# Performance work log

Measured on AMD Instinct MI355X. Metric: run time of the kernel, lower is better.

## Reference

```python
import jax, jax.numpy as jnp
import numpy as np

HUGE = 1e9  # stand-in for ops.HUGE_INT


def setup_inputs() -> dict:
    key = jax.random.key(0)
    ks = jax.random.split(key, 8)
    B, Q, K = 8, 128, 256
    Dq = Dk = Dv = H = 512
    query = jax.random.normal(ks[0], (B, Q, Dq), dtype=jnp.float32)
    k_ = jax.random.normal(ks[1], (B, K, Dk), dtype=jnp.float32)
    value = jax.random.normal(ks[2], (B, K, Dv), dtype=jnp.float32)
    mask = jax.random.randint(ks[3], (B, K), 0, 2, dtype=jnp.int32)
    # FFN params: linear1 (Dq+Dk -> H, bias), linear2 (H -> 1, no bias)
    W1 = jax.random.normal(ks[4], (Dq + Dk, H), dtype=jnp.float32) * 0.05
    b1 = jax.random.normal(ks[5], (H,), dtype=jnp.float32) * 0.05
    w2 = jax.random.normal(ks[6], (H, 1), dtype=jnp.float32) * 0.05
    return {"query": query, "key": k_, "value": value, "mask": mask,
            "W1": W1, "b1": b1, "w2": w2}


def reference(query, key, value, mask, W1, b1, w2):
    # Additive (FFN) attention. Original tiles query/key into [B, Q*K, Dq+Dk]
    # and applies linear1; concat@W1 is separable, so we project q and k
    # separately and broadcast-add (same math, no tiled concat tensor).
    Dq = query.shape[-1]
    Wq, Wk = W1[:Dq], W1[Dq:]
    q_proj = jnp.einsum('bqd,dh->bqh', query, Wq)   # [B,Q,H]
    k_proj = jnp.einsum('bkd,dh->bkh', key, Wk)     # [B,K,H]
    hidden = jnp.tanh(q_proj[:, :, None, :] + k_proj[:, None, :, :] + b1)  # [B,Q,K,H]
    scores = jnp.einsum('bqkh,h->bqk', hidden, w2[:, 0])  # [B,Q,K]
    # padding mask fill BEFORE scaling, matching the original op order
    scores = jnp.where(mask[:, None, :] != 0, -HUGE, scores)
    scores = scores / jnp.sqrt(jnp.float32(key.shape[-1]))
    attn_weights = jax.nn.softmax(scores, axis=-1)
    attn_vec = jnp.einsum('bqk,bkv->bqv', attn_weights, value)  # dropout=0 at eval
    return attn_vec, attn_weights
```

## Files before the change

### kernel.cpp

```cpp
#include <hip/hip_runtime.h>
#include <hip/hip_bf16.h>

#define B_ 8
#define Q_ 128
#define K_ 256
#define D_ 512
#define TWOLOG2E 2.8853900817779268f
#define SCALE 0.044194173824159216f
#define L2E 1.4426950408889634f
#define MASKVAL (-44194173.824159216f)

typedef __attribute__((ext_vector_type(8))) short frag8;
typedef __attribute__((ext_vector_type(4))) float f32x4;

__device__ __forceinline__ float fexp2(float x) {
  float r;
  asm("v_exp_f32 %0, %1" : "=v"(r) : "v"(x));
  return r;
}
__device__ __forceinline__ float frcp(float x) {
  float r;
  asm("v_rcp_f32 %0, %1" : "=v"(r) : "v"(x));
  return r;
}
__device__ __forceinline__ unsigned f2bf_u(float x) {
  unsigned u = __float_as_uint(x);
  return (u + 0x7FFFu + ((u >> 16) & 1u)) >> 16;
}
__device__ __forceinline__ unsigned short f2bf(float x) {
  return (unsigned short)f2bf_u(x);
}
__device__ __forceinline__ unsigned packbf(float lo, float hi) {
  return f2bf_u(lo) | (f2bf_u(hi) << 16);
}

__global__ __launch_bounds__(256) void gemm_kernel(
    const float* __restrict__ query, const float* __restrict__ key,
    const float* __restrict__ W1, const float* __restrict__ b1,
    float* __restrict__ qp, float* __restrict__ kpbT) {
  __shared__ short As[32 * 64];
  __shared__ short Bs[64 * 72];
  const int t = threadIdx.x;
  const int m0 = blockIdx.y * 32;
  const int n0 = blockIdx.x * 64;
  const bool is_k = (m0 >= B_ * Q_);
  const float* X = is_k ? key : query;
  const int xrow0 = is_k ? (m0 - B_ * Q_) : m0;
  const float* Wb = W1 + (is_k ? (size_t)D_ * D_ : 0);

  const int am = t >> 3;
  const int ac = t & 7;
  const float* gA = X + (size_t)(xrow0 + am) * D_ + ac * 8;
  short* aw = As + am * 64 + ((ac ^ (am & 7)) * 8);

  const int prow = t >> 4;
  const int n4 = (t & 15) * 4;
  const float* gB = Wb + n0 + n4;

  const int l = t & 63;
  const int w = t >> 6;
  const int lr = l & 15;
  const int kg = l >> 4;
  const int key8 = lr & 7;
  int aoff[2][2], boff[2];
#pragma unroll
  for (int kk = 0; kk < 2; ++kk) {
    const int cposA = ((kg + kk * 4) ^ key8) * 8;
#pragma unroll
    for (int mt = 0; mt < 2; ++mt) aoff[mt][kk] = (mt * 16 + lr) * 64 + cposA;
    boff[kk] = (w * 16 + lr) * 72 + (kg + kk * 4) * 8;
  }

  f32x4 acc[2];
  acc[0] = (f32x4){0.f, 0.f, 0.f, 0.f};
  acc[1] = (f32x4){0.f, 0.f, 0.f, 0.f};

  for (int k0 = 0; k0 < D_; k0 += 64) {
    float4 a0 = *(const float4*)(gA + k0);
    float4 a1 = *(const float4*)(gA + k0 + 4);
    float4 w00 = *(const float4*)(gB + (size_t)(k0 + 2 * prow) * D_);
    float4 w01 = *(const float4*)(gB + (size_t)(k0 + 2 * prow + 1) * D_);
    float4 w10 = *(const float4*)(gB + (size_t)(k0 + 2 * prow + 32) * D_);
    float4 w11 = *(const float4*)(gB + (size_t)(k0 + 2 * prow + 33) * D_);
    __syncthreads();
    {
      union { frag8 f; unsigned short u[8]; } av;
      av.u[0] = f2bf(a0.x); av.u[1] = f2bf(a0.y); av.u[2] = f2bf(a0.z); av.u[3] = f2bf(a0.w);
      av.u[4] = f2bf(a1.x); av.u[5] = f2bf(a1.y); av.u[6] = f2bf(a1.z); av.u[7] = f2bf(a1.w);
      *(frag8*)aw = av.f;
    }
    {
      float lo0[4] = {w00.x, w00.y, w00.z, w00.w};
      float hi0[4] = {w01.x, w01.y, w01.z, w01.w};
      float lo1[4] = {w10.x, w10.y, w10.z, w10.w};
      float hi1[4] = {w11.x, w11.y, w11.z, w11.w};
#pragma unroll
      for (int j = 0; j < 4; ++j) {
        *(unsigned*)(Bs + (n4 + j) * 72 + 2 * prow) = packbf(lo0[j], hi0[j]);
        *(unsigned*)(Bs + (n4 + j) * 72 + 2 * (prow + 16)) = packbf(lo1[j], hi1[j]);
      }
    }
    __syncthreads();
#pragma unroll
    for (int kk = 0; kk < 2; ++kk) {
      frag8 bf = *(const frag8*)(Bs + boff[kk]);
#pragma unroll
      for (int mt = 0; mt < 2; ++mt) {
        frag8 af = *(const frag8*)(As + aoff[mt][kk]);
        acc[mt] = __builtin_amdgcn_mfma_f32_16x16x32_bf16(af, bf, acc[mt], 0, 0, 0);
      }
    }
  }

  const int col = n0 + w * 16 + lr;
  if (is_k) {
    const float bc = b1[col];
#pragma unroll
    for (int mt = 0; mt < 2; ++mt) {
      const int krow = m0 - B_ * Q_ + mt * 16 + kg * 4;
      const int bb = krow >> 8;
      const int kk0 = krow & 255;
      float4 v;
      v.x = fexp2((acc[mt][0] + bc) * TWOLOG2E);
      v.y = fexp2((acc[mt][1] + bc) * TWOLOG2E);
      v.z = fexp2((acc[mt][2] + bc) * TWOLOG2E);
      v.w = fexp2((acc[mt][3] + bc) * TWOLOG2E);
      *(float4*)&kpbT[((size_t)bb * D_ + col) * K_ + kk0] = v;
    }
  } else {
#pragma unroll
    for (int mt = 0; mt < 2; ++mt) {
#pragma unroll
      for (int i = 0; i < 4; ++i) {
        const int row = m0 + mt * 16 + kg * 4 + i;
        qp[(size_t)row * D_ + col] = fexp2(acc[mt][i] * TWOLOG2E);
      }
    }
  }
}

__global__ __launch_bounds__(1024) void attn_kernel(
    const float* __restrict__ qp, const float* __restrict__ kpbT,
    const float* __restrict__ value, const int* __restrict__ mask,
    const float* __restrict__ w2,
    float* __restrict__ out_vec, float* __restrict__ out_w) {
  __shared__ float smem_p[16 * 512];
  __shared__ float pw[4 * 256];
  const int bid = blockIdx.x;
  const int b = bid & 7;
  const int q0 = (bid >> 3) * 4;
  const int t = threadIdx.x;
  const int lane = t & 63;
  const int w = __builtin_amdgcn_readfirstlane(t >> 6);
  const int kc = w & 1;
  const int hq = w >> 1;
  const int h0 = hq * 64;

  {
    const float* pk = kpbT + ((size_t)b * D_ + h0) * K_ + kc * 128 + 2 * lane;
    const float* q_0 = qp + (size_t)(b * Q_ + q0 + 0) * D_ + h0;
    const float* q_1 = qp + (size_t)(b * Q_ + q0 + 1) * D_ + h0;
    const float* q_2 = qp + (size_t)(b * Q_ + q0 + 2) * D_ + h0;
    const float* q_3 = qp + (size_t)(b * Q_ + q0 + 3) * D_ + h0;
    const float* w2h = w2 + h0;

    float2 a0 = {0.f, 0.f}, a1 = {0.f, 0.f}, a2 = {0.f, 0.f}, a3 = {0.f, 0.f};
    for (int h = 0; h < 64; h += 8) {
      float2 kv[8];
#pragma unroll
      for (int j = 0; j < 8; ++j) kv[j] = *(const float2*)&pk[(size_t)(h + j) * K_];
      float4 e0a = *(const float4*)(q_0 + h), e0b = *(const float4*)(q_0 + h + 4);
      float4 e1a = *(const float4*)(q_1 + h), e1b = *(const float4*)(q_1 + h + 4);
      float4 e2a = *(const float4*)(q_2 + h), e2b = *(const float4*)(q_2 + h + 4);
      float4 e3a = *(const float4*)(q_3 + h), e3b = *(const float4*)(q_3 + h + 4);
      float4 wa = *(const float4*)(w2h + h), wb = *(const float4*)(w2h + h + 4);
      float E0[8] = {e0a.x, e0a.y, e0a.z, e0a.w, e0b.x, e0b.y, e0b.z, e0b.w};
      float E1[8] = {e1a.x, e1a.y, e1a.z, e1a.w, e1b.x, e1b.y, e1b.z, e1b.w};
      float E2[8] = {e2a.x, e2a.y, e2a.z, e2a.w, e2b.x, e2b.y, e2b.z, e2b.w};
      float E3[8] = {e3a.x, e3a.y, e3a.z, e3a.w, e3b.x, e3b.y, e3b.z, e3b.w};
      float WV[8] = {wa.x, wa.y, wa.z, wa.w, wb.x, wb.y, wb.z, wb.w};
#pragma unroll
      for (int j = 0; j < 8; ++j) {
        a0.x = fmaf(WV[j], frcp(fmaf(E0[j], kv[j].x, 1.f)), a0.x);
        a0.y = fmaf(WV[j], frcp(fmaf(E0[j], kv[j].y, 1.f)), a0.y);
        a1.x = fmaf(WV[j], frcp(fmaf(E1[j], kv[j].x, 1.f)), a1.x);
        a1.y = fmaf(WV[j], frcp(fmaf(E1[j], kv[j].y, 1.f)), a1.y);
        a2.x = fmaf(WV[j], frcp(fmaf(E2[j], kv[j].x, 1.f)), a2.x);
        a2.y = fmaf(WV[j], frcp(fmaf(E2[j], kv[j].y, 1.f)), a2.y);
        a3.x = fmaf(WV[j], frcp(fmaf(E3[j], kv[j].x, 1.f)), a3.x);
        a3.y = fmaf(WV[j], frcp(fmaf(E3[j], kv[j].y, 1.f)), a3.y);
      }
    }
    *(float2*)&smem_p[w * 512 + 0 * 128 + 2 * lane] = a0;
    *(float2*)&smem_p[w * 512 + 1 * 128 + 2 * lane] = a1;
    *(float2*)&smem_p[w * 512 + 2 * 128 + 2 * lane] = a2;
    *(float2*)&smem_p[w * 512 + 3 * 128 + 2 * lane] = a3;
  }
  __syncthreads();

  if (w < 4) {
    const int q = w;
    float sw = 0.f;
#pragma unroll
    for (int m = 0; m < 8; ++m) sw += w2[lane + 64 * m];
#pragma unroll
    for (int off = 32; off; off >>= 1) sw += __shfl_xor(sw, off);

    float s[4];
#pragma unroll
    for (int r = 0; r < 4; ++r) {
      const int kcc = r >> 1;
      const int off = (r & 1) * 64 + lane;
      float p = 0.f;
#pragma unroll
      for (int hh = 0; hh < 8; ++hh)
        p += smem_p[(hh * 2 + kcc) * 512 + q * 128 + off];
      const int mk = mask[b * K_ + r * 64 + lane];
      s[r] = mk ? MASKVAL : fmaf(-2.f, p, sw) * SCALE;
    }
    float mx = fmaxf(fmaxf(s[0], s[1]), fmaxf(s[2], s[3]));
#pragma unroll
    for (int off = 32; off; off >>= 1) mx = fmaxf(mx, __shfl_xor(mx, off));
    float e[4], sum = 0.f;
#pragma unroll
    for (int r = 0; r < 4; ++r) {
      e[r] = fexp2((s[r] - mx) * L2E);
      sum += e[r];
    }
#pragma unroll
    for (int off = 32; off; off >>= 1) sum += __shfl_xor(sum, off);
    const float inv = frcp(sum);
    float* ow = out_w + (size_t)(b * Q_ + q0 + q) * K_;
#pragma unroll
    for (int r = 0; r < 4; ++r) {
      const float p = e[r] * inv;
      pw[q * 256 + r * 64 + lane] = p;
      ow[r * 64 + lane] = p;
    }
  }
  __syncthreads();

  const int col = t & 511;
  const int qq = t >> 9;
  float o0 = 0.f, o1 = 0.f;
  const float* vb = value + (size_t)b * K_ * D_;
  for (int k = 0; k < K_; k += 4) {
    const float4 p0 = *(const float4*)&pw[(qq * 2 + 0) * 256 + k];
    const float4 p1 = *(const float4*)&pw[(qq * 2 + 1) * 256 + k];
    const float v0 = vb[(size_t)(k + 0) * D_ + col];
    const float v1 = vb[(size_t)(k + 1) * D_ + col];
    const float v2 = vb[(size_t)(k + 2) * D_ + col];
    const float v3 = vb[(size_t)(k + 3) * D_ + col];
    o0 = fmaf(p0.x, v0, fmaf(p0.y, v1, fmaf(p0.z, v2, fmaf(p0.w, v3, o0))));
    o1 = fmaf(p1.x, v0, fmaf(p1.y, v1, fmaf(p1.z, v2, fmaf(p1.w, v3, o1))));
  }
  out_vec[(size_t)(b * Q_ + q0 + qq * 2 + 0) * D_ + col] = o0;
  out_vec[(size_t)(b * Q_ + q0 + qq * 2 + 1) * D_ + col] = o1;
}

extern "C" void kernel_launch(void* const* d_in, const int* in_sizes, int n_in,
                              void* d_out, int out_size, void* d_ws, size_t ws_size,
                              hipStream_t stream) {
  const float* query = (const float*)d_in[0];
  const float* key   = (const float*)d_in[1];
  const float* value = (const float*)d_in[2];
  const int*   mask  = (const int*)d_in[3];
  const float* W1    = (const float*)d_in[4];
  const float* b1    = (const float*)d_in[5];
  const float* w2    = (const float*)d_in[6];

  float* out_vec = (float*)d_out;
  float* out_w   = out_vec + (size_t)B_ * Q_ * D_;

  float* qp   = (float*)d_ws;
  float* kpbT = qp + (size_t)B_ * Q_ * D_;

  gemm_kernel<<<dim3(8, 96), 256, 0, stream>>>(query, key, W1, b1, qp, kpbT);
  attn_kernel<<<dim3(256), 1024, 0, stream>>>(qp, kpbT, value, mask, w2,
                                              out_vec, out_w);
}
```

Baseline: 113.8 us.

## Split PV reduction over K across thread groups with shared-memory partial sums

The attention-times-value stage now gives each thread 2 columns and all 4 query rows over a quarter of the K range, instead of 1 column and 2 rows over the full K. Each value load is reused across 4 rows and the loop is 4x shorter. Partial sums are written to shared memory and reduced by a second pass. This costs an extra barrier and shared-memory traffic, and it reuses the smem_p buffer, which is why a barrier is placed before the writes.

```diff
diff --git a/kernel.cpp b/kernel.cpp
--- a/kernel.cpp
+++ b/kernel.cpp
@@ -240,22 +240,51 @@
   }
   __syncthreads();
 
-  const int col = t & 511;
-  const int qq = t >> 9;
-  float o0 = 0.f, o1 = 0.f;
-  const float* vb = value + (size_t)b * K_ * D_;
-  for (int k = 0; k < K_; k += 4) {
-    const float4 p0 = *(const float4*)&pw[(qq * 2 + 0) * 256 + k];
-    const float4 p1 = *(const float4*)&pw[(qq * 2 + 1) * 256 + k];
-    const float v0 = vb[(size_t)(k + 0) * D_ + col];
-    const float v1 = vb[(size_t)(k + 1) * D_ + col];
-    const float v2 = vb[(size_t)(k + 2) * D_ + col];
-    const float v3 = vb[(size_t)(k + 3) * D_ + col];
-    o0 = fmaf(p0.x, v0, fmaf(p0.y, v1, fmaf(p0.z, v2, fmaf(p0.w, v3, o0))));
-    o1 = fmaf(p1.x, v0, fmaf(p1.y, v1, fmaf(p1.z, v2, fmaf(p1.w, v3, o1))));
-  }
-  out_vec[(size_t)(b * Q_ + q0 + qq * 2 + 0) * D_ + col] = o0;
-  out_vec[(size_t)(b * Q_ + q0 + qq * 2 + 1) * D_ + col] = o1;
+  {
+    const int cp = t & 255;
+    const int col = cp * 2;
+    const int kq = t >> 8;
+    const float* vb = value + (size_t)b * K_ * D_ + (size_t)(kq * 64) * D_ + col;
+    const float* pwq = pw + kq * 64;
+
+    float2 o0 = {0.f, 0.f}, o1 = {0.f, 0.f}, o2 = {0.f, 0.f}, o3 = {0.f, 0.f};
+    for (int k0 = 0; k0 < 64; k0 += 4) {
+      const float4 P0 = *(const float4*)&pwq[0 * 256 + k0];
+      const float4 P1 = *(const float4*)&pwq[1 * 256 + k0];
+      const float4 P2 = *(const float4*)&pwq[2 * 256 + k0];
+      const float4 P3 = *(const float4*)&pwq[3 * 256 + k0];
+      const float2 v0 = *(const float2*)&vb[(size_t)(k0 + 0) * D_];
+      const float2 v1 = *(const float2*)&vb[(size_t)(k0 + 1) * D_];
+      const float2 v2 = *(const float2*)&vb[(size_t)(k0 + 2) * D_];
+      const float2 v3 = *(const float2*)&vb[(size_t)(k0 + 3) * D_];
+      o0.x = fmaf(P0.x, v0.x, fmaf(P0.y, v1.x, fmaf(P0.z, v2.x, fmaf(P0.w, v3.x, o0.x))));
+      o0.y = fmaf(P0.x, v0.y, fmaf(P0.y, v1.y, fmaf(P0.z, v2.y, fmaf(P0.w, v3.y, o0.y))));
+      o1.x = fmaf(P1.x, v0.x, fmaf(P1.y, v1.x, fmaf(P1.z, v2.x, fmaf(P1.w, v3.x, o1.x))));
+      o1.y = fmaf(P1.x, v0.y, fmaf(P1.y, v1.y, fmaf(P1.z, v2.y, fmaf(P1.w, v3.y, o1.y))));
+      o2.x = fmaf(P2.x, v0.x, fmaf(P2.y, v1.x, fmaf(P2.z, v2.x, fmaf(P2.w, v3.x, o2.x))));
+      o2.y = fmaf(P2.x, v0.y, fmaf(P2.y, v1.y, fmaf(P2.z, v2.y, fmaf(P2.w, v3.y, o2.y))));
+      o3.x = fmaf(P3.x, v0.x, fmaf(P3.y, v1.x, fmaf(P3.z, v2.x, fmaf(P3.w, v3.x, o3.x))));
+      o3.y = fmaf(P3.x, v0.y, fmaf(P3.y, v1.y, fmaf(P3.z, v2.y, fmaf(P3.w, v3.y, o3.y))));
+    }
+    __syncthreads();
+    *(float2*)&smem_p[kq * 2048 + 0 * 512 + col] = o0;
+    *(float2*)&smem_p[kq * 2048 + 1 * 512 + col] = o1;
+    *(float2*)&smem_p[kq * 2048 + 2 * 512 + col] = o2;
+    *(float2*)&smem_p[kq * 2048 + 3 * 512 + col] = o3;
+  }
+  __syncthreads();
+
+  {
+#pragma unroll
+    for (int rep = 0; rep < 2; ++rep) {
+      const int idx = t + rep * 1024;
+      const int q = idx >> 9;
+      const int c = idx & 511;
+      const float s = smem_p[0 * 2048 + q * 512 + c] + smem_p[1 * 2048 + q * 512 + c] +
+                      smem_p[2 * 2048 + q * 512 + c] + smem_p[3 * 2048 + q * 512 + c];
+      out_vec[(size_t)(b * Q_ + q0 + q) * D_ + c] = s;
+    }
+  }
 }
 
 extern "C" void kernel_launch(void* const* d_in, const int* in_sizes, int n_in,
```

Result: faster. 111.1 us (-2.3%).
